# Kernel optimization log

Hardware: AMD Instinct MI355X
Metric: run time of the kernel (lower is better)

The kernel has to match this reference:

```python
import jax, jax.numpy as jnp
import numpy as np

# Model dims (match init_kwargs / Mamba2 defaults)
D_MODEL = 1024
D_STATE = 128
D_CONV = 4
EXPAND = 2
HEADDIM = 64
NGROUPS = 1
D_INNER = EXPAND * D_MODEL            # 2048
NHEADS = D_INNER // HEADDIM           # 32
D_IN_PROJ = 2 * D_INNER + 2 * NGROUPS * D_STATE + NHEADS  # 4384 (d_mlp == 0)
CONV_DIM = D_INNER + 2 * NGROUPS * D_STATE                 # 2304
BATCH = 2
SEQLEN = 512
EPS = 1e-5


def _silu(x):
    return x * jax.nn.sigmoid(x)


def setup_inputs() -> dict:
    key = jax.random.key(0)
    ks = jax.random.split(key, 8)
    u = jax.random.normal(ks[0], (BATCH, SEQLEN, D_MODEL), jnp.float32)
    W_in = jax.random.normal(ks[1], (D_IN_PROJ, D_MODEL), jnp.float32) * (D_MODEL ** -0.5)
    conv_w = jax.random.normal(ks[2], (CONV_DIM, 1, D_CONV), jnp.float32) * (D_CONV ** -0.5)
    conv_b = jnp.zeros((CONV_DIM,), jnp.float32)
    # dt_bias init as in the torch module (inverse-softplus of dt in [dt_min, dt_max])
    dt = jnp.exp(jax.random.uniform(ks[3], (NHEADS,), jnp.float32)
                 * (np.log(0.1) - np.log(0.001)) + np.log(0.001))
    dt = jnp.clip(dt, 1e-4, None)
    dt_bias = dt + jnp.log(-jnp.expm1(-dt))
    A_log = jnp.log(jax.random.uniform(ks[4], (NHEADS,), jnp.float32, minval=1.0, maxval=16.0))
    D_param = jnp.ones((NHEADS,), jnp.float32)
    norm_w = jnp.ones((D_INNER,), jnp.float32)
    W_out = jax.random.normal(ks[5], (D_MODEL, D_INNER), jnp.float32) * (D_INNER ** -0.5)
    return dict(u=u, W_in=W_in, conv_w=conv_w, conv_b=conv_b, dt_bias=dt_bias,
                A_log=A_log, D_param=D_param, norm_w=norm_w, W_out=W_out)


def reference(u, W_in, conv_w, conv_b, dt_bias, A_log, D_param, norm_w, W_out):
    B, L, _ = u.shape
    # in_proj (no bias): [B,L,d_in_proj]
    zxbcdt = jnp.einsum('bld,ed->ble', u, W_in)
    z = zxbcdt[..., :D_INNER]
    xBC = zxbcdt[..., D_INNER:D_INNER + CONV_DIM]
    dt = zxbcdt[..., D_INNER + CONV_DIM:]          # [B,L,H]

    # causal depthwise conv1d (pad left d_conv-1 == conv padding + slice in torch)
    xc = jnp.transpose(xBC, (0, 2, 1))             # [B,C,L]
    xc = jax.lax.conv_general_dilated(
        xc, conv_w, window_strides=(1,), padding=[(D_CONV - 1, 0)],
        dimension_numbers=('NCH', 'OIH', 'NCH'), feature_group_count=CONV_DIM)
    xc = xc + conv_b[None, :, None]
    xBC = _silu(jnp.transpose(xc, (0, 2, 1)))      # [B,L,C]

    x = xBC[..., :D_INNER].reshape(B, L, NHEADS, HEADDIM)
    Bv = xBC[..., D_INNER:D_INNER + NGROUPS * D_STATE].reshape(B, L, NGROUPS, D_STATE)
    Cv = xBC[..., D_INNER + NGROUPS * D_STATE:].reshape(B, L, NGROUPS, D_STATE)

    A = -jnp.exp(A_log)                            # [H]
    dt = jax.nn.softplus(dt + dt_bias)             # [B,L,H]

    def step(state, inp):
        dt_t, x_t, B_t, C_t = inp                  # [B,H],[B,H,P],[B,G,N],[B,G,N]
        dA = jnp.exp(dt_t * A)                     # [B,H]
        dBx = jnp.einsum('bh,bgn,bhp->bhpn', dt_t, B_t, x_t)
        state = state * dA[:, :, None, None] + dBx
        y = jnp.einsum('bhpn,bgn->bhp', state, C_t) + D_param[:, None] * x_t
        return state, y

    state0 = jnp.zeros((B, NHEADS, HEADDIM, D_STATE), u.dtype)
    xs = (jnp.moveaxis(dt, 1, 0), jnp.moveaxis(x, 1, 0),
          jnp.moveaxis(Bv, 1, 0), jnp.moveaxis(Cv, 1, 0))
    _, ys = jax.lax.scan(step, state0, xs)         # ys: [L,B,H,P]
    y = jnp.moveaxis(ys, 0, 1).reshape(B, L, D_INNER)

    # RMSNormGated, norm_before_gate=False: gate first, then rmsnorm
    yg = y * _silu(z)
    yn = yg * jax.lax.rsqrt(jnp.mean(yg * yg, axis=-1, keepdims=True) + EPS) * norm_w

    return jnp.einsum('bld,ed->ble', yn, W_out)    # out_proj, no bias
```

## Files before the change

### kernel.cpp

```cpp
#include <hip/hip_runtime.h>
#include <hip/hip_bf16.h>

#define D_MODEL   1024
#define D_STATE   128
#define D_INNER   2048
#define NHEADS    32
#define HEADDIM   64
#define D_IN_PROJ 4384
#define NPROJ_PAD 4480
#define CONV_DIM  2304
#define BATCH     2
#define SEQLEN    512
#define M_TOKENS  (BATCH*SEQLEN)
#define EPS       1e-5f
#define LC        64
#define NCH       (SEQLEN/LC)

typedef __bf16 bf16x8 __attribute__((ext_vector_type(8)));
typedef float  f32x4  __attribute__((ext_vector_type(4)));

__device__ __forceinline__ ushort f2bf(float f) {
  union { float f; unsigned int i; } v; v.f = f;
  unsigned int x = v.i;
  return (ushort)((x + 0x7fffu + ((x >> 16) & 1u)) >> 16);
}
__device__ __forceinline__ float bf2f(ushort u) {
  union { unsigned int i; float f; } v; v.i = ((unsigned int)u) << 16; return v.f;
}

__device__ __forceinline__ void gload_lds16u(const ushort* g, ushort* l) {
  __builtin_amdgcn_global_load_lds(
      (const __attribute__((address_space(1))) void*)g,
      (__attribute__((address_space(3))) void*)l, 16, 0, 0);
}

__device__ __forceinline__ void cvt8(const float* __restrict__ s,
                                     ushort* __restrict__ d, int i) {
  const float4 a = *(const float4*)(s + i);
  const float4 b = *(const float4*)(s + i + 4);
  uint4 v;
  v.x = (unsigned)f2bf(a.x) | ((unsigned)f2bf(a.y) << 16);
  v.y = (unsigned)f2bf(a.z) | ((unsigned)f2bf(a.w) << 16);
  v.z = (unsigned)f2bf(b.x) | ((unsigned)f2bf(b.y) << 16);
  v.w = (unsigned)f2bf(b.z) | ((unsigned)f2bf(b.w) << 16);
  *(uint4*)(d + i) = v;
}
__global__ __launch_bounds__(256) void cvt3(const float* __restrict__ s0, ushort* __restrict__ d0, int n0,
                                            const float* __restrict__ s1, ushort* __restrict__ d1, int n1,
                                            const float* __restrict__ s2, ushort* __restrict__ d2, int n2,
                                            const float* __restrict__ nw) {
  const int i = (blockIdx.x * 256 + threadIdx.x) * 8;
  if (i < n0)           cvt8(s0, d0, i);
  else if (i < n0 + n1) cvt8(s1, d1, i - n0);
  else if (i < n0 + n1 + n2) {
    const int j = i - n0 - n1;
    const int k = j & (D_INNER - 1);
    const float4 a = *(const float4*)(s2 + j);
    const float4 b = *(const float4*)(s2 + j + 4);
    const float4 wa = *(const float4*)(nw + k);
    const float4 wb = *(const float4*)(nw + k + 4);
    uint4 v;
    v.x = (unsigned)f2bf(a.x * wa.x) | ((unsigned)f2bf(a.y * wa.y) << 16);
    v.y = (unsigned)f2bf(a.z * wa.z) | ((unsigned)f2bf(a.w * wa.w) << 16);
    v.z = (unsigned)f2bf(b.x * wb.x) | ((unsigned)f2bf(b.y * wb.y) << 16);
    v.w = (unsigned)f2bf(b.z * wb.z) | ((unsigned)f2bf(b.w * wb.w) << 16);
    *(uint4*)(d2 + j) = v;
  }
}

template <int BM, int BN, int MASK_N>
__global__ __launch_bounds__(256) void gemm_tile(const ushort* __restrict__ A,
                                                 const ushort* __restrict__ Bt,
                                                 float* __restrict__ C,
                                                 int Nreal, int K, int ldc) {
  constexpr int WM = BM / 2, WN = BN / 2, FM = WM / 16, FN = WN / 16;
  constexpr int LA = BM * 4 / 256, LB = BN * 4 / 256;
  __shared__ ushort As[2 * BM * 32];
  __shared__ ushort Bs[2 * BN * 32];
  const int tid = threadIdx.x, lane = tid & 63, wave = tid >> 6;
  const int r16 = lane & 15, q = lane >> 4;
  const int wm = wave & 1, wn = wave >> 1;
  const int m0 = blockIdx.y * BM, n0 = blockIdx.x * BN;

  f32x4 acc[FM][FN] = {};

  for (int k0 = 0; k0 < K; k0 += 64) {
    __syncthreads();
    #pragma unroll
    for (int pp = 0; pp < 2; ++pp) {
      #pragma unroll
      for (int it = 0; it < LA; ++it) {
        const int idx = it * 256 + tid;
        gload_lds16u(A + (size_t)(m0 + (idx >> 2)) * K + k0 + pp * 32 + (idx & 3) * 8,
                     As + pp * BM * 32 + (it * 256 + wave * 64) * 8);
      }
      #pragma unroll
      for (int it = 0; it < LB; ++it) {
        const int idx = it * 256 + tid;
        gload_lds16u(Bt + (size_t)(n0 + (idx >> 2)) * K + k0 + pp * 32 + (idx & 3) * 8,
                     Bs + pp * BN * 32 + (it * 256 + wave * 64) * 8);
      }
    }
    __syncthreads();

    #pragma unroll
    for (int pp = 0; pp < 2; ++pp) {
      bf16x8 af[FM], bfr[FN];
      #pragma unroll
      for (int i = 0; i < FM; ++i)
        af[i] = *(const bf16x8*)(const void*)(As + pp * BM * 32 + (wm * WM + i * 16 + r16) * 32 + q * 8);
      #pragma unroll
      for (int j = 0; j < FN; ++j)
        bfr[j] = *(const bf16x8*)(const void*)(Bs + pp * BN * 32 + (wn * WN + j * 16 + r16) * 32 + q * 8);
      #pragma unroll
      for (int i = 0; i < FM; ++i)
        #pragma unroll
        for (int j = 0; j < FN; ++j)
          acc[i][j] = __builtin_amdgcn_mfma_f32_16x16x32_bf16(af[i], bfr[j], acc[i][j], 0, 0, 0);
    }
  }

  #pragma unroll
  for (int i = 0; i < FM; ++i) {
    const int row = m0 + wm * WM + i * 16 + q * 4;
    #pragma unroll
    for (int j = 0; j < FN; ++j) {
      const int col = n0 + wn * WN + j * 16 + r16;
      if (!MASK_N || col < Nreal) {
        #pragma unroll
        for (int r = 0; r < 4; ++r)
          C[(size_t)(row + r) * ldc + col] = acc[i][j][r];
      }
    }
  }
}

__global__ __launch_bounds__(256) void gemm_sk(const ushort* __restrict__ A,
                                               const ushort* __restrict__ Bt,
                                               float* __restrict__ C,
                                               const float* __restrict__ sumsq,
                                               int Khalf, int ldab, int ldc) {
  __shared__ ushort As[2 * 64 * 32];
  __shared__ ushort Bs[2 * 64 * 32];
  const int tid = threadIdx.x, lane = tid & 63, wave = tid >> 6;
  const int r16 = lane & 15, q = lane >> 4;
  const int wm = wave & 1, wn = wave >> 1;
  const int m0 = blockIdx.y * 64, n0 = blockIdx.x * 64;
  const int kb = blockIdx.z * Khalf;

  f32x4 acc[2][2] = {};
  for (int k0 = 0; k0 < Khalf; k0 += 64) {
    __syncthreads();
    #pragma unroll
    for (int pp = 0; pp < 2; ++pp) {
      gload_lds16u(A + (size_t)(m0 + (tid >> 2)) * ldab + kb + k0 + pp * 32 + (tid & 3) * 8,
                   As + pp * 64 * 32 + (tid & ~63) * 8);
      gload_lds16u(Bt + (size_t)(n0 + (tid >> 2)) * ldab + kb + k0 + pp * 32 + (tid & 3) * 8,
                   Bs + pp * 64 * 32 + (tid & ~63) * 8);
    }
    __syncthreads();

    #pragma unroll
    for (int pp = 0; pp < 2; ++pp) {
      bf16x8 af[2], bfr[2];
      #pragma unroll
      for (int i = 0; i < 2; ++i)
        af[i] = *(const bf16x8*)(const void*)(As + pp * 64 * 32 + (wm * 32 + i * 16 + r16) * 32 + q * 8);
      #pragma unroll
      for (int j = 0; j < 2; ++j)
        bfr[j] = *(const bf16x8*)(const void*)(Bs + pp * 64 * 32 + (wn * 32 + j * 16 + r16) * 32 + q * 8);
      #pragma unroll
      for (int i = 0; i < 2; ++i)
        #pragma unroll
        for (int j = 0; j < 2; ++j)
          acc[i][j] = __builtin_amdgcn_mfma_f32_16x16x32_bf16(af[i], bfr[j], acc[i][j], 0, 0, 0);
    }
  }

  #pragma unroll
  for (int i = 0; i < 2; ++i) {
    const int row = m0 + wm * 32 + i * 16 + q * 4;
    float rms[4];
    #pragma unroll
    for (int r = 0; r < 4; ++r)
      rms[r] = rsqrtf(sumsq[row + r] * (1.f / D_INNER) + EPS);
    #pragma unroll
    for (int j = 0; j < 2; ++j) {
      const int col = n0 + wn * 32 + j * 16 + r16;
      #pragma unroll
      for (int r = 0; r < 4; ++r)
        unsafeAtomicAdd(&C[(size_t)(row + r) * ldc + col], acc[i][j][r] * rms[r]);
    }
  }
}

__global__ __launch_bounds__(256) void conv_dt(const float* __restrict__ zx,
                                               const float* __restrict__ cw,
                                               const float* __restrict__ cb,
                                               float* __restrict__ xbc,
                                               ushort* __restrict__ BCbf,
                                               const float* __restrict__ dt_bias,
                                               const float* __restrict__ A_log,
                                               float* __restrict__ dts,
                                               float* __restrict__ csum) {
  const int blk = blockIdx.x;
  if (blk < 1152) {
    const int g  = blk / 9;
    const int c  = (blk % 9) * 256 + threadIdx.x;
    const int b  = g >> 6;
    const int t0 = (g & 63) * 8;
    const float4 w4 = *(const float4*)(cw + c * 4);
    const float bias = cb[c];
    const float* col = zx + (size_t)(b * SEQLEN) * D_IN_PROJ + D_INNER + c;
    float win[11];
    #pragma unroll
    for (int k = 0; k < 11; ++k) {
      const int t = t0 - 3 + k;
      win[k] = (t >= 0) ? col[(size_t)t * D_IN_PROJ] : 0.f;
    }
    #pragma unroll
    for (int i = 0; i < 8; ++i) {
      float a = bias;
      a = fmaf(win[i],     w4.x, a);
      a = fmaf(win[i + 1], w4.y, a);
      a = fmaf(win[i + 2], w4.z, a);
      a = fmaf(win[i + 3], w4.w, a);
      const float s = a / (1.f + __expf(-a));
      const size_t bt = (size_t)(b * SEQLEN + t0 + i);
      xbc[bt * CONV_DIM + c] = s;
      if (c >= D_INNER) BCbf[bt * 256 + (c - D_INNER)] = f2bf(s);
    }
  } else {
    const int bh = blk - 1152;
    const int b = bh >> 5, h = bh & 31;
    const int wave = threadIdx.x >> 6, lane = threadIdx.x & 63;
    const float dtb = dt_bias[h];
    const float An  = -__expf(A_log[h]);
    for (int cc = wave; cc < NCH; cc += 4) {
      const int t = cc * LC + lane;
      const float raw = zx[(size_t)(b * SEQLEN + t) * D_IN_PROJ + (D_INNER + CONV_DIM) + h] + dtb;
      const float sp = (raw > 20.f) ? raw : log1pf(__expf(raw));
      float x = sp * An;
      #pragma unroll
      for (int off = 1; off < 64; off <<= 1) {
        const float v = __shfl_up(x, off);
        if (lane >= off) x += v;
      }
      dts[(size_t)bh * SEQLEN + t]  = sp;
      csum[(size_t)bh * SEQLEN + t] = x;
    }
  }
}

__global__ __launch_bounds__(256) void chunk_intra(const float* __restrict__ xbc,
                                                   const ushort* __restrict__ BCbf,
                                                   const float* __restrict__ dts,
                                                   const float* __restrict__ csum,
                                                   ushort* __restrict__ Yi,
                                                   ushort* __restrict__ dS) {
  const int blk = blockIdx.x;
  const int c = blk & 7, h = (blk >> 3) & 31, b = blk >> 8;
  const int bh = b * 32 + h;
  const int tid = threadIdx.x, lane = tid & 63, wave = tid >> 6;
  const int r16 = lane & 15, q = lane >> 4;

  __shared__ ushort Ml[64 * 72];
  __shared__ ushort Xt[64 * 72];
  __shared__ ushort Bw[128 * 72];
  __shared__ float dtl[LC], csl[LC];

  if (tid < LC) {
    dtl[tid] = dts[(size_t)bh * SEQLEN + c * LC + tid];
    csl[tid] = csum[(size_t)bh * SEQLEN + c * LC + tid];
  }
  __syncthreads();
  const float cs63 = csl[LC - 1];

  const ushort* Cp = BCbf + (size_t)(b * SEQLEN + c * LC + wave * 16 + r16) * 256 + 128 + q * 8;
  const ushort* Bp = BCbf + (size_t)(b * SEQLEN + c * LC + r16) * 256 + q * 8;
  f32x4 g[4] = {};
  #pragma unroll
  for (int kk = 0; kk < 4; ++kk) {
    const bf16x8 a = *(const bf16x8*)(const void*)(Cp + kk * 32);
    #pragma unroll
    for (int j = 0; j < 4; ++j) {
      const bf16x8 bb = *(const bf16x8*)(const void*)(Bp + (size_t)j * 16 * 256 + kk * 32);
      g[j] = __builtin_amdgcn_mfma_f32_16x16x32_bf16(a, bb, g[j], 0, 0, 0);
    }
  }
  float cst[4];
  #pragma unroll
  for (int r = 0; r < 4; ++r) cst[r] = csl[wave * 16 + q * 4 + r];
  #pragma unroll
  for (int j = 0; j < 4; ++j) {
    const int s = j * 16 + r16;
    const float ds_ = dtl[s], css = csl[s];
    #pragma unroll
    for (int r = 0; r < 4; ++r) {
      const int t = wave * 16 + q * 4 + r;
      const float v = (s <= t) ? g[j][r] * ds_ * __expf(cst[r] - css) : 0.f;
      Ml[t * 72 + s] = f2bf(v);
    }
  }

  const float* xb = xbc + (size_t)(b * SEQLEN + c * LC) * CONV_DIM + h * HEADDIM;
  #pragma unroll
  for (int i = 0; i < 16; ++i) {
    const int idx = i * 256 + tid;
    const int s = idx >> 6, p = idx & 63;
    Xt[p * 72 + s] = f2bf(xb[(size_t)s * CONV_DIM + p]);
  }
  const float* Bb = xbc + (size_t)(b * SEQLEN + c * LC) * CONV_DIM + D_INNER;
  #pragma unroll
  for (int i = 0; i < 32; ++i) {
    const int idx = i * 256 + tid;
    const int s = idx >> 7, n = idx & 127;
    const float w = dtl[s] * __expf(cs63 - csl[s]);
    Bw[n * 72 + s] = f2bf(Bb[(size_t)s * CONV_DIM + n] * w);
  }
  __syncthreads();

  f32x4 accY[4] = {};
  f32x4 accS[2][4] = {};
  #pragma unroll
  for (int kk = 0; kk < 2; ++kk) {
    const bf16x8 am = *(const bf16x8*)(const void*)(Ml + (wave * 16 + r16) * 72 + kk * 32 + q * 8);
    const bf16x8 a0 = *(const bf16x8*)(const void*)(Bw + (wave * 32 + r16) * 72 + kk * 32 + q * 8);
    const bf16x8 a1 = *(const bf16x8*)(const void*)(Bw + (wave * 32 + 16 + r16) * 72 + kk * 32 + q * 8);
    #pragma unroll
    for (int j = 0; j < 4; ++j) {
      const bf16x8 bx = *(const bf16x8*)(const void*)(Xt + (j * 16 + r16) * 72 + kk * 32 + q * 8);
      accY[j]    = __builtin_amdgcn_mfma_f32_16x16x32_bf16(am, bx, accY[j], 0, 0, 0);
      accS[0][j] = __builtin_amdgcn_mfma_f32_16x16x32_bf16(a0, bx, accS[0][j], 0, 0, 0);
      accS[1][j] = __builtin_amdgcn_mfma_f32_16x16x32_bf16(a1, bx, accS[1][j], 0, 0, 0);
    }
  }

  ushort* Yp = Yi + (size_t)blk * 4096;
  #pragma unroll
  for (int j = 0; j < 4; ++j)
    #pragma unroll
    for (int r = 0; r < 4; ++r)
      Yp[(wave * 16 + q * 4 + r) * 64 + j * 16 + r16] = f2bf(accY[j][r]);

  ushort* Sp = dS + (size_t)blk * 8192;
  #pragma unroll
  for (int u = 0; u < 2; ++u)
    #pragma unroll
    for (int j = 0; j < 4; ++j)
      #pragma unroll
      for (int r = 0; r < 4; ++r)
        Sp[(wave * 32 + u * 16 + q * 4 + r) * 64 + j * 16 + r16] = f2bf(accS[u][j][r]);
}

__global__ __launch_bounds__(256) void chunk_inter(const ushort* __restrict__ BCbf,
                                                   const ushort* __restrict__ dS,
                                                   const ushort* __restrict__ Yi,
                                                   const float* __restrict__ xbc,
                                                   const float* __restrict__ zx,
                                                   const float* __restrict__ csum,
                                                   const float* __restrict__ Dp,
                                                   ushort* __restrict__ yn,
                                                   float* __restrict__ sumsq) {
  const int blk = blockIdx.x;
  const int c = blk & 7, h = (blk >> 3) & 31, b = blk >> 8;
  const int bh = b * 32 + h;
  const int tid = threadIdx.x, lane = tid & 63, wave = tid >> 6;
  const int r16 = lane & 15, q = lane >> 4;

  __shared__ ushort Stile[64 * 132];

  const int p  = tid & 63;
  const int n0 = (tid >> 6) * 32;
  float S[32] = {};
  float w = 1.f;
  for (int cp = c - 1; cp >= 0; --cp) {
    const ushort* dp = dS + ((size_t)bh * 8 + cp) * 8192 + (size_t)n0 * 64 + p;
    #pragma unroll
    for (int j = 0; j < 32; ++j)
      S[j] = fmaf(w, bf2f(dp[(size_t)j * 64]), S[j]);
    w *= __expf(csum[(size_t)bh * SEQLEN + cp * LC + (LC - 1)]);
  }
  #pragma unroll
  for (int j = 0; j < 16; ++j) {
    const unsigned v = (unsigned)f2bf(S[2 * j]) | ((unsigned)f2bf(S[2 * j + 1]) << 16);
    *(unsigned*)&Stile[p * 132 + n0 + 2 * j] = v;
  }
  __syncthreads();

  const ushort* Cp = BCbf + (size_t)(b * SEQLEN + c * LC + wave * 16 + r16) * 256 + 128 + q * 8;
  f32x4 acc[4] = {};
  #pragma unroll
  for (int kk = 0; kk < 4; ++kk) {
    const bf16x8 a = *(const bf16x8*)(const void*)(Cp + kk * 32);
    #pragma unroll
    for (int j = 0; j < 4; ++j) {
      const bf16x8 bb = *(const bf16x8*)(const void*)(Stile + (j * 16 + r16) * 132 + kk * 32 + q * 8);
      acc[j] = __builtin_amdgcn_mfma_f32_16x16x32_bf16(a, bb, acc[j], 0, 0, 0);
    }
  }

  const float Dh = Dp[h];
  const ushort* Yp = Yi + (size_t)blk * 4096;
  float sc[4], ssq[4] = {0.f, 0.f, 0.f, 0.f};
  #pragma unroll
  for (int r = 0; r < 4; ++r)
    sc[r] = __expf(csum[(size_t)bh * SEQLEN + c * LC + wave * 16 + q * 4 + r]);
  #pragma unroll
  for (int j = 0; j < 4; ++j) {
    const int col = j * 16 + r16;
    #pragma unroll
    for (int r = 0; r < 4; ++r) {
      const int t = wave * 16 + q * 4 + r;
      const size_t row = (size_t)(b * SEQLEN + c * LC + t);
      const float xv = xbc[row * CONV_DIM + h * HEADDIM + col];
      const float yv = acc[j][r] * sc[r] + bf2f(Yp[t * 64 + col]) + Dh * xv;
      const float z  = zx[row * D_IN_PROJ + h * HEADDIM + col];
      const float yg = yv * (z / (1.f + __expf(-z)));
      yn[row * D_INNER + h * HEADDIM + col] = f2bf(yg);
      ssq[r] = fmaf(yg, yg, ssq[r]);
    }
  }
  #pragma unroll
  for (int o = 1; o < 16; o <<= 1) {
    #pragma unroll
    for (int r = 0; r < 4; ++r) ssq[r] += __shfl_xor(ssq[r], o);
  }
  if (r16 == 0) {
    #pragma unroll
    for (int r = 0; r < 4; ++r) {
      const int t = wave * 16 + q * 4 + r;
      unsafeAtomicAdd(&sumsq[b * SEQLEN + c * LC + t], ssq[r]);
    }
  }
}

extern "C" void kernel_launch(void* const* d_in, const int* in_sizes, int n_in,
                              void* d_out, int out_size, void* d_ws, size_t ws_size,
                              hipStream_t stream) {
  const float* u       = (const float*)d_in[0];
  const float* W_in    = (const float*)d_in[1];
  const float* conv_w  = (const float*)d_in[2];
  const float* conv_b  = (const float*)d_in[3];
  const float* dt_bias = (const float*)d_in[4];
  const float* A_log   = (const float*)d_in[5];
  const float* D_par   = (const float*)d_in[6];
  const float* norm_w  = (const float*)d_in[7];
  const float* W_out   = (const float*)d_in[8];
  float* out = (float*)d_out;

  char* ws = (char*)d_ws;
  float*  zx      = (float*)ws;
  float*  xbc     = (float*)(ws + 17956864);
  float*  sumsq   = (float*)(ws + 27394048);
  ushort* yn      = (ushort*)(ws + 35782656);
  ushort* u_bf    = (ushort*)(ws + 39976960);
  ushort* Win_bf  = (ushort*)(ws + 42074112);
  ushort* Yi      = (ushort*)(ws + 39976960);
  ushort* Wout_bf = (ushort*)(ws + 51052544);
  ushort* BC_bf   = (ushort*)(ws + 55246848);
  float*  dts     = (float*)(ws + 55771136);
  float*  csum    = (float*)(ws + 55902208);
  ushort* dS      = (ushort*)(ws + 56295424);

  hipMemsetAsync(out, 0, (size_t)M_TOKENS * D_MODEL * sizeof(float), stream);
  hipMemsetAsync(sumsq, 0, (size_t)M_TOKENS * sizeof(float), stream);

  const int n_u = M_TOKENS * D_MODEL, n_wi = D_IN_PROJ * D_MODEL, n_wo = D_MODEL * D_INNER;
  cvt3<<<(n_u + n_wi + n_wo) / (256 * 8), 256, 0, stream>>>(
      u, u_bf, n_u, W_in, Win_bf, n_wi, W_out, Wout_bf, n_wo, norm_w);

  gemm_tile<128, 64, 1><<<dim3(NPROJ_PAD / 64, M_TOKENS / 128), 256, 0, stream>>>(
      u_bf, Win_bf, zx, D_IN_PROJ, D_MODEL, D_IN_PROJ);
  conv_dt<<<1152 + 64, 256, 0, stream>>>(zx, conv_w, conv_b, xbc, BC_bf,
                                         dt_bias, A_log, dts, csum);

  chunk_intra<<<BATCH * NHEADS * NCH, 256, 0, stream>>>(xbc, BC_bf, dts, csum, Yi, dS);
  chunk_inter<<<BATCH * NHEADS * NCH, 256, 0, stream>>>(BC_bf, dS, Yi, xbc, zx,
                                                        csum, D_par, yn, sumsq);

  gemm_sk<<<dim3(D_MODEL / 64, M_TOKENS / 64, 2), 256, 0, stream>>>(
      yn, Wout_bf, out, sumsq, D_INNER / 2, D_INNER, D_MODEL);
}
```

Measured before the change: 171.5 us.

## Store intermediates as bf16, fold memsets into convert kernel, deepen GEMM K-steps

The in-projection GEMM now writes bf16 instead of fp32, and the conv output xbc is stored in bf16. The separate B/C bf16 buffer is dropped; downstream kernels read B/C directly from xbc. The two memsets are folded into the conversion kernel as extra zero-fill ranges, saving launches. Both GEMMs also load 128 K-elements per sync instead of 64, cutting barrier count at the cost of more LDS, while z, x and dt lose precision from bf16 rounding.

```diff
diff --git a/kernel.cpp b/kernel.cpp
--- a/kernel.cpp
+++ b/kernel.cpp
@@ -45,10 +45,12 @@
   v.w = (unsigned)f2bf(b.z) | ((unsigned)f2bf(b.w) << 16);
   *(uint4*)(d + i) = v;
 }
-__global__ __launch_bounds__(256) void cvt3(const float* __restrict__ s0, ushort* __restrict__ d0, int n0,
-                                            const float* __restrict__ s1, ushort* __restrict__ d1, int n1,
-                                            const float* __restrict__ s2, ushort* __restrict__ d2, int n2,
-                                            const float* __restrict__ nw) {
+__global__ __launch_bounds__(256) void cvt3z(const float* __restrict__ s0, ushort* __restrict__ d0, int n0,
+                                             const float* __restrict__ s1, ushort* __restrict__ d1, int n1,
+                                             const float* __restrict__ s2, ushort* __restrict__ d2, int n2,
+                                             const float* __restrict__ nw,
+                                             float* __restrict__ zout, int n3,
+                                             float* __restrict__ zsum, int n4) {
   const int i = (blockIdx.x * 256 + threadIdx.x) * 8;
   if (i < n0)           cvt8(s0, d0, i);
   else if (i < n0 + n1) cvt8(s1, d1, i - n0);
@@ -65,18 +67,28 @@
     v.z = (unsigned)f2bf(b.x * wb.x) | ((unsigned)f2bf(b.y * wb.y) << 16);
     v.w = (unsigned)f2bf(b.z * wb.z) | ((unsigned)f2bf(b.w * wb.w) << 16);
     *(uint4*)(d2 + j) = v;
-  }
-}
-
-template <int BM, int BN, int MASK_N>
+  } else if (i < n0 + n1 + n2 + n3) {
+    const int j = i - n0 - n1 - n2;
+    const float4 z = {0.f, 0.f, 0.f, 0.f};
+    *(float4*)(zout + j) = z;
+    *(float4*)(zout + j + 4) = z;
+  } else if (i < n0 + n1 + n2 + n3 + n4) {
+    const int j = i - n0 - n1 - n2 - n3;
+    const float4 z = {0.f, 0.f, 0.f, 0.f};
+    *(float4*)(zsum + j) = z;
+    *(float4*)(zsum + j + 4) = z;
+  }
+}
+
+template <int BM, int BN, int PK>
 __global__ __launch_bounds__(256) void gemm_tile(const ushort* __restrict__ A,
                                                  const ushort* __restrict__ Bt,
-                                                 float* __restrict__ C,
+                                                 ushort* __restrict__ C,
                                                  int Nreal, int K, int ldc) {
   constexpr int WM = BM / 2, WN = BN / 2, FM = WM / 16, FN = WN / 16;
   constexpr int LA = BM * 4 / 256, LB = BN * 4 / 256;
-  __shared__ ushort As[2 * BM * 32];
-  __shared__ ushort Bs[2 * BN * 32];
+  __shared__ ushort As[PK * BM * 32];
+  __shared__ ushort Bs[PK * BN * 32];
   const int tid = threadIdx.x, lane = tid & 63, wave = tid >> 6;
   const int r16 = lane & 15, q = lane >> 4;
   const int wm = wave & 1, wn = wave >> 1;
@@ -84,10 +96,10 @@
 
   f32x4 acc[FM][FN] = {};
 
-  for (int k0 = 0; k0 < K; k0 += 64) {
+  for (int k0 = 0; k0 < K; k0 += 32 * PK) {
     __syncthreads();
     #pragma unroll
-    for (int pp = 0; pp < 2; ++pp) {
+    for (int pp = 0; pp < PK; ++pp) {
       #pragma unroll
       for (int it = 0; it < LA; ++it) {
         const int idx = it * 256 + tid;
@@ -104,7 +116,7 @@
     __syncthreads();
 
     #pragma unroll
-    for (int pp = 0; pp < 2; ++pp) {
+    for (int pp = 0; pp < PK; ++pp) {
       bf16x8 af[FM], bfr[FN];
       #pragma unroll
       for (int i = 0; i < FM; ++i)
@@ -126,10 +138,10 @@
     #pragma unroll
     for (int j = 0; j < FN; ++j) {
       const int col = n0 + wn * WN + j * 16 + r16;
-      if (!MASK_N || col < Nreal) {
+      if (col < Nreal) {
         #pragma unroll
         for (int r = 0; r < 4; ++r)
-          C[(size_t)(row + r) * ldc + col] = acc[i][j][r];
+          C[(size_t)(row + r) * ldc + col] = f2bf(acc[i][j][r]);
       }
     }
   }
@@ -140,8 +152,8 @@
                                                float* __restrict__ C,
                                                const float* __restrict__ sumsq,
                                                int Khalf, int ldab, int ldc) {
-  __shared__ ushort As[2 * 64 * 32];
-  __shared__ ushort Bs[2 * 64 * 32];
+  __shared__ ushort As[4 * 64 * 32];
+  __shared__ ushort Bs[4 * 64 * 32];
   const int tid = threadIdx.x, lane = tid & 63, wave = tid >> 6;
   const int r16 = lane & 15, q = lane >> 4;
   const int wm = wave & 1, wn = wave >> 1;
@@ -149,10 +161,10 @@
   const int kb = blockIdx.z * Khalf;
 
   f32x4 acc[2][2] = {};
-  for (int k0 = 0; k0 < Khalf; k0 += 64) {
+  for (int k0 = 0; k0 < Khalf; k0 += 128) {
     __syncthreads();
     #pragma unroll
-    for (int pp = 0; pp < 2; ++pp) {
+    for (int pp = 0; pp < 4; ++pp) {
       gload_lds16u(A + (size_t)(m0 + (tid >> 2)) * ldab + kb + k0 + pp * 32 + (tid & 3) * 8,
                    As + pp * 64 * 32 + (tid & ~63) * 8);
       gload_lds16u(Bt + (size_t)(n0 + (tid >> 2)) * ldab + kb + k0 + pp * 32 + (tid & 3) * 8,
@@ -161,7 +173,7 @@
     __syncthreads();
 
     #pragma unroll
-    for (int pp = 0; pp < 2; ++pp) {
+    for (int pp = 0; pp < 4; ++pp) {
       bf16x8 af[2], bfr[2];
       #pragma unroll
       for (int i = 0; i < 2; ++i)
@@ -194,11 +206,10 @@
   }
 }
 
-__global__ __launch_bounds__(256) void conv_dt(const float* __restrict__ zx,
+__global__ __launch_bounds__(256) void conv_dt(const ushort* __restrict__ zx,
                                                const float* __restrict__ cw,
                                                const float* __restrict__ cb,
-                                               float* __restrict__ xbc,
-                                               ushort* __restrict__ BCbf,
+                                               ushort* __restrict__ xbc,
                                                const float* __restrict__ dt_bias,
                                                const float* __restrict__ A_log,
                                                float* __restrict__ dts,
@@ -211,12 +222,12 @@
     const int t0 = (g & 63) * 8;
     const float4 w4 = *(const float4*)(cw + c * 4);
     const float bias = cb[c];
-    const float* col = zx + (size_t)(b * SEQLEN) * D_IN_PROJ + D_INNER + c;
+    const ushort* col = zx + (size_t)(b * SEQLEN) * D_IN_PROJ + D_INNER + c;
     float win[11];
     #pragma unroll
     for (int k = 0; k < 11; ++k) {
       const int t = t0 - 3 + k;
-      win[k] = (t >= 0) ? col[(size_t)t * D_IN_PROJ] : 0.f;
+      win[k] = (t >= 0) ? bf2f(col[(size_t)t * D_IN_PROJ]) : 0.f;
     }
     #pragma unroll
     for (int i = 0; i < 8; ++i) {
@@ -226,9 +237,7 @@
       a = fmaf(win[i + 2], w4.z, a);
       a = fmaf(win[i + 3], w4.w, a);
       const float s = a / (1.f + __expf(-a));
-      const size_t bt = (size_t)(b * SEQLEN + t0 + i);
-      xbc[bt * CONV_DIM + c] = s;
-      if (c >= D_INNER) BCbf[bt * 256 + (c - D_INNER)] = f2bf(s);
+      xbc[(size_t)(b * SEQLEN + t0 + i) * CONV_DIM + c] = f2bf(s);
     }
   } else {
     const int bh = blk - 1152;
@@ -238,7 +247,7 @@
     const float An  = -__expf(A_log[h]);
     for (int cc = wave; cc < NCH; cc += 4) {
       const int t = cc * LC + lane;
-      const float raw = zx[(size_t)(b * SEQLEN + t) * D_IN_PROJ + (D_INNER + CONV_DIM) + h] + dtb;
+      const float raw = bf2f(zx[(size_t)(b * SEQLEN + t) * D_IN_PROJ + (D_INNER + CONV_DIM) + h]) + dtb;
       const float sp = (raw > 20.f) ? raw : log1pf(__expf(raw));
       float x = sp * An;
       #pragma unroll
@@ -252,8 +261,7 @@
   }
 }
 
-__global__ __launch_bounds__(256) void chunk_intra(const float* __restrict__ xbc,
-                                                   const ushort* __restrict__ BCbf,
+__global__ __launch_bounds__(256) void chunk_intra(const ushort* __restrict__ xbc,
                                                    const float* __restrict__ dts,
                                                    const float* __restrict__ csum,
                                                    ushort* __restrict__ Yi,
@@ -276,15 +284,16 @@
   __syncthreads();
   const float cs63 = csl[LC - 1];
 
-  const ushort* Cp = BCbf + (size_t)(b * SEQLEN + c * LC + wave * 16 + r16) * 256 + 128 + q * 8;
-  const ushort* Bp = BCbf + (size_t)(b * SEQLEN + c * LC + r16) * 256 + q * 8;
+  const ushort* rowbase = xbc + (size_t)(b * SEQLEN + c * LC) * CONV_DIM;
+  const ushort* Cp = rowbase + (size_t)(wave * 16 + r16) * CONV_DIM + D_INNER + 128 + q * 8;
+  const ushort* Bp = rowbase + (size_t)r16 * CONV_DIM + D_INNER + q * 8;
   f32x4 g[4] = {};
   #pragma unroll
   for (int kk = 0; kk < 4; ++kk) {
     const bf16x8 a = *(const bf16x8*)(const void*)(Cp + kk * 32);
     #pragma unroll
     for (int j = 0; j < 4; ++j) {
-      const bf16x8 bb = *(const bf16x8*)(const void*)(Bp + (size_t)j * 16 * 256 + kk * 32);
+      const bf16x8 bb = *(const bf16x8*)(const void*)(Bp + (size_t)j * 16 * CONV_DIM + kk * 32);
       g[j] = __builtin_amdgcn_mfma_f32_16x16x32_bf16(a, bb, g[j], 0, 0, 0);
     }
   }
@@ -303,20 +312,20 @@
     }
   }
 
-  const float* xb = xbc + (size_t)(b * SEQLEN + c * LC) * CONV_DIM + h * HEADDIM;
+  const ushort* xb = rowbase + h * HEADDIM;
   #pragma unroll
   for (int i = 0; i < 16; ++i) {
     const int idx = i * 256 + tid;
     const int s = idx >> 6, p = idx & 63;
-    Xt[p * 72 + s] = f2bf(xb[(size_t)s * CONV_DIM + p]);
-  }
-  const float* Bb = xbc + (size_t)(b * SEQLEN + c * LC) * CONV_DIM + D_INNER;
+    Xt[p * 72 + s] = xb[(size_t)s * CONV_DIM + p];
+  }
+  const ushort* Bb = rowbase + D_INNER;
   #pragma unroll
   for (int i = 0; i < 32; ++i) {
     const int idx = i * 256 + tid;
     const int s = idx >> 7, n = idx & 127;
     const float w = dtl[s] * __expf(cs63 - csl[s]);
-    Bw[n * 72 + s] = f2bf(Bb[(size_t)s * CONV_DIM + n] * w);
+    Bw[n * 72 + s] = f2bf(bf2f(Bb[(size_t)s * CONV_DIM + n]) * w);
   }
   __syncthreads();
 
@@ -353,11 +362,10 @@
         Sp[(wave * 32 + u * 16 + q * 4 + r) * 64 + j * 16 + r16] = f2bf(accS[u][j][r]);
 }
 
-__global__ __launch_bounds__(256) void chunk_inter(const ushort* __restrict__ BCbf,
+__global__ __launch_bounds__(256) void chunk_inter(const ushort* __restrict__ xbc,
                                                    const ushort* __restrict__ dS,
                                                    const ushort* __restrict__ Yi,
-                                                   const float* __restrict__ xbc,
-                                                   const float* __restrict__ zx,
+                                                   const ushort* __restrict__ zx,
                                                    const float* __restrict__ csum,
                                                    const float* __restrict__ Dp,
                                                    ushort* __restrict__ yn,
@@ -388,7 +396,8 @@
   }
   __syncthreads();
 
-  const ushort* Cp = BCbf + (size_t)(b * SEQLEN + c * LC + wave * 16 + r16) * 256 + 128 + q * 8;
+  const ushort* rowbase = xbc + (size_t)(b * SEQLEN + c * LC) * CONV_DIM;
+  const ushort* Cp = rowbase + (size_t)(wave * 16 + r16) * CONV_DIM + D_INNER + 128 + q * 8;
   f32x4 acc[4] = {};
   #pragma unroll
   for (int kk = 0; kk < 4; ++kk) {
@@ -413,9 +422,9 @@
     for (int r = 0; r < 4; ++r) {
       const int t = wave * 16 + q * 4 + r;
       const size_t row = (size_t)(b * SEQLEN + c * LC + t);
-      const float xv = xbc[row * CONV_DIM + h * HEADDIM + col];
+      const float xv = bf2f(xbc[row * CONV_DIM + h * HEADDIM + col]);
       const float yv = acc[j][r] * sc[r] + bf2f(Yp[t * 64 + col]) + Dh * xv;
-      const float z  = zx[row * D_IN_PROJ + h * HEADDIM + col];
+      const float z  = bf2f(zx[row * D_IN_PROJ + h * HEADDIM + col]);
       const float yg = yv * (z / (1.f + __expf(-z)));
       yn[row * D_INNER + h * HEADDIM + col] = f2bf(yg);
       ssq[r] = fmaf(yg, yg, ssq[r]);
@@ -450,33 +459,32 @@
   float* out = (float*)d_out;
 
   char* ws = (char*)d_ws;
-  float*  zx      = (float*)ws;
-  float*  xbc     = (float*)(ws + 17956864);
-  float*  sumsq   = (float*)(ws + 27394048);
-  ushort* yn      = (ushort*)(ws + 35782656);
-  ushort* u_bf    = (ushort*)(ws + 39976960);
-  ushort* Win_bf  = (ushort*)(ws + 42074112);
-  ushort* Yi      = (ushort*)(ws + 39976960);
-  ushort* Wout_bf = (ushort*)(ws + 51052544);
-  ushort* BC_bf   = (ushort*)(ws + 55246848);
-  float*  dts     = (float*)(ws + 55771136);
-  float*  csum    = (float*)(ws + 55902208);
-  ushort* dS      = (ushort*)(ws + 56295424);
-
-  hipMemsetAsync(out, 0, (size_t)M_TOKENS * D_MODEL * sizeof(float), stream);
-  hipMemsetAsync(sumsq, 0, (size_t)M_TOKENS * sizeof(float), stream);
+  ushort* zx      = (ushort*)ws;
+  ushort* xbc     = (ushort*)(ws + 8978432);
+  float*  sumsq   = (float*)(ws + 13697024);
+  ushort* yn      = (ushort*)(ws + 13701120);
+  ushort* u_bf    = (ushort*)(ws + 17895424);
+  ushort* Win_bf  = (ushort*)(ws + 19992576);
+  ushort* Yi      = (ushort*)(ws + 17895424);
+  ushort* Wout_bf = (ushort*)(ws + 28971008);
+  float*  dts     = (float*)(ws + 33165312);
+  float*  csum    = (float*)(ws + 33296384);
+  ushort* dS      = (ushort*)(ws + 33427456);
 
   const int n_u = M_TOKENS * D_MODEL, n_wi = D_IN_PROJ * D_MODEL, n_wo = D_MODEL * D_INNER;
-  cvt3<<<(n_u + n_wi + n_wo) / (256 * 8), 256, 0, stream>>>(
-      u, u_bf, n_u, W_in, Win_bf, n_wi, W_out, Wout_bf, n_wo, norm_w);
-
-  gemm_tile<128, 64, 1><<<dim3(NPROJ_PAD / 64, M_TOKENS / 128), 256, 0, stream>>>(
+  const int n_out = M_TOKENS * D_MODEL, n_ss = M_TOKENS;
+  const int n_tot = n_u + n_wi + n_wo + n_out + n_ss;
+  cvt3z<<<(n_tot + 2047) / 2048, 256, 0, stream>>>(
+      u, u_bf, n_u, W_in, Win_bf, n_wi, W_out, Wout_bf, n_wo, norm_w,
+      out, n_out, sumsq, n_ss);
+
+  gemm_tile<128, 64, 4><<<dim3(NPROJ_PAD / 64, M_TOKENS / 128), 256, 0, stream>>>(
       u_bf, Win_bf, zx, D_IN_PROJ, D_MODEL, D_IN_PROJ);
-  conv_dt<<<1152 + 64, 256, 0, stream>>>(zx, conv_w, conv_b, xbc, BC_bf,
+  conv_dt<<<1152 + 64, 256, 0, stream>>>(zx, conv_w, conv_b, xbc,
                                          dt_bias, A_log, dts, csum);
 
-  chunk_intra<<<BATCH * NHEADS * NCH, 256, 0, stream>>>(xbc, BC_bf, dts, csum, Yi, dS);
-  chunk_inter<<<BATCH * NHEADS * NCH, 256, 0, stream>>>(BC_bf, dS, Yi, xbc, zx,
+  chunk_intra<<<BATCH * NHEADS * NCH, 256, 0, stream>>>(xbc, dts, csum, Yi, dS);
+  chunk_inter<<<BATCH * NHEADS * NCH, 256, 0, stream>>>(xbc, dS, Yi, zx,
                                                         csum, D_par, yn, sumsq);
 
   gemm_sk<<<dim3(D_MODEL / 64, M_TOKENS / 64, 2), 256, 0, stream>>>(
```

Result: faster. 164.2 us (median of 2 runs) (-4.3%).
